# Kernel tuning notes

Hardware: AMD Instinct MI355X
Metric: run time of the kernel (lower is better)

Reference implementation:

```python
import jax, jax.numpy as jnp
import numpy as np

N = 100000        # num_nodes
W_IN = 256        # input feature dim
W_OUT = 64        # args.node_dim
C = 2             # args.num_channels
T = 4             # num_edge_type
E = 800000        # edges per edge type
NUM_CLASS = 4
M = 20000         # number of target nodes
BETA = 0.5        # args.beta


def setup_inputs() -> dict:
    key = jax.random.key(0)
    ks = jax.random.split(key, 10)
    X = jax.random.normal(ks[0], (N, W_IN), dtype=jnp.float32)
    edge_index = jax.random.randint(ks[1], (T, 2, E), 0, N)
    edge_value = jax.random.uniform(ks[2], (T, E), dtype=jnp.float32)
    target_x = jax.random.randint(ks[3], (M,), 0, N)
    target = jax.random.randint(ks[4], (M,), 0, NUM_CLASS)
    # learned params
    Ws = jax.random.normal(ks[5], (C, W_IN, W_OUT), dtype=jnp.float32) * 0.05   # GCNConv weights
    conv_weight = jax.random.normal(ks[6], (C, T), dtype=jnp.float32) * 0.1     # FastGTConv.weight
    linear1_W = jax.random.normal(ks[7], (W_OUT, W_OUT * C), dtype=jnp.float32) * 0.05
    linear1_b = jnp.zeros((W_OUT,), dtype=jnp.float32)
    lin_W = jax.random.normal(ks[8], (NUM_CLASS, W_OUT), dtype=jnp.float32) * 0.05
    lin_b = jnp.zeros((NUM_CLASS,), dtype=jnp.float32)
    return dict(X=X, edge_value=edge_value, Ws=Ws, conv_weight=conv_weight,
                linear1_W=linear1_W, linear1_b=linear1_b, lin_W=lin_W, lin_b=lin_b,
                edge_index=edge_index, target_x=target_x, target=target)


def reference(X, edge_value, Ws, conv_weight, linear1_W, linear1_b, lin_W, lin_b,
              edge_index, target_x, target):
    # FastGTConv: softmax over edge types per channel
    filt = jax.nn.softmax(conv_weight, axis=1)            # [C, T]
    rows = edge_index[:, 0, :].reshape(-1)                # [T*E]
    cols = edge_index[:, 1, :].reshape(-1)                # [T*E]
    # X_ = H = [X @ W_c for each channel]
    X_ = jnp.einsum('nd,cdo->cno', X, Ws)                 # [C, N, W_OUT]
    outs = []
    for c in range(C):
        # concat+coalesce(add) then spmm == scatter-add of weighted messages
        vals = (edge_value * filt[c][:, None]).reshape(-1)       # [T*E]
        msgs = vals[:, None] * X_[c][cols]                        # [T*E, W_OUT]
        Hc = jax.ops.segment_sum(msgs, rows, num_segments=N)      # [N, W_OUT]
        outs.append(jax.nn.relu(BETA * X_[c] + (1.0 - BETA) * Hc))
    H_ = jnp.concatenate(outs, axis=1)                    # [N, C*W_OUT]
    H_ = jax.nn.relu(H_ @ linear1_W.T + linear1_b)        # [N, W_OUT]
    y = H_[target_x] @ lin_W.T + lin_b                    # [M, NUM_CLASS]
    logp = jax.nn.log_softmax(y, axis=-1)
    loss = -jnp.mean(jnp.take_along_axis(logp, target[:, None], axis=1))
    return loss, y
```

## Files before the change

kernel.cpp:

```cpp
#include <hip/hip_runtime.h>

#define N_NODES 100000
#define W_INF   256
#define W_OUTF  64
#define C_CH    2
#define T_ET    4
#define E_EDGE  800000
#define NUM_CLS 4
#define M_TGT   20000
#define BETA    0.5f
#define MAXDEG  96

typedef __attribute__((ext_vector_type(8))) short bf16x8;
typedef __attribute__((ext_vector_type(4))) float floatx4;

__device__ inline short f2bf(float f) {
    unsigned u = __builtin_bit_cast(unsigned, f);
    u += 0x7FFF + ((u >> 16) & 1);
    return (short)(u >> 16);
}
__device__ inline float bflo(unsigned q) { return __builtin_bit_cast(float, q << 16); }
__device__ inline float bfhi(unsigned q) { return __builtin_bit_cast(float, q & 0xFFFF0000u); }

__global__ void setup_kernel(const float* __restrict__ Ws,
                             const float* __restrict__ conv_weight,
                             const int* __restrict__ target_x,
                             short* __restrict__ Bt, float* __restrict__ filt,
                             int* __restrict__ rid, int* __restrict__ nrows,
                             float* __restrict__ out) {
    int i = blockIdx.x * 256 + threadIdx.x;
    if (i == 0) { *nrows = 0; out[0] = 0.f; }
    if (i < C_CH) {
        int c = i;
        float mx = -1e30f;
        for (int t = 0; t < T_ET; t++) mx = fmaxf(mx, conv_weight[c * T_ET + t]);
        float e[T_ET];
        float s = 0.f;
        for (int t = 0; t < T_ET; t++) { e[t] = expf(conv_weight[c * T_ET + t] - mx); s += e[t]; }
        for (int t = 0; t < T_ET; t++) filt[c * T_ET + t] = e[t] / s;
    }
    if (i < C_CH * W_OUTF * W_INF) {
        int co = i >> 8, k = i & 255;
        int c = co >> 6, o = co & 63;
        Bt[i] = f2bf(Ws[((size_t)c * W_INF + k) * W_OUTF + o]);
    }
    if (i < M_TGT) rid[target_x[i]] = -2;
}

__global__ void compact_kernel(int* __restrict__ rid, int* __restrict__ row_list,
                               int* __restrict__ nrows, int* __restrict__ counts) {
    int n = blockIdx.x * blockDim.x + threadIdx.x;
    if (n < M_TGT) counts[n] = 0;
    int lane = threadIdx.x & 63;
    bool flag = (n < N_NODES) && (rid[n] == -2);
    unsigned long long mask = __ballot(flag);
    int base = 0;
    if (lane == 0 && mask) base = atomicAdd(nrows, __popcll(mask));
    base = __shfl(base, 0);
    if (flag) {
        int id = base + __popcll(mask & ((1ULL << lane) - 1ULL));
        rid[n] = id;
        row_list[id] = n;
    }
}

#define GMT  64
#define BLDA2 136
#define GEMM_NB  ((N_NODES + GMT - 1) / GMT)
#define BUILD_BX ((E_EDGE / 8 + 255) / 256)
#define BUILD_TOT (BUILD_BX * T_ET)
__global__ __launch_bounds__(256, 5)
void fused_gemm_build(const float* __restrict__ X, const short* __restrict__ Bt,
                      short* __restrict__ Xp,
                      const int* __restrict__ edge_index,
                      const float* __restrict__ edge_value,
                      const int* __restrict__ rid,
                      int* __restrict__ counts,
                      unsigned long long* __restrict__ records) {
    __shared__ short Bl[64][BLDA2];
    int tid = threadIdx.x;
    int bx = blockIdx.x;
    if ((bx & 1) == 0) {
        int g = bx >> 1;
        if (g >= GEMM_NB) return;
        int w = tid >> 6, lane = tid & 63;
        int quad = lane >> 4, l15 = lane & 15;
        int m0 = g * GMT + w * 16;
        int arow = m0 + l15;
        if (arow >= N_NODES) arow = N_NODES - 1;
        const float* xrow = X + (size_t)arow * W_INF;
        floatx4 acc[C_CH][4] = {};
        #pragma unroll 1
        for (int kh = 0; kh < 2; kh++) {
            bf16x8 af[4];
            #pragma unroll
            for (int kc = 0; kc < 4; kc++) {
                int kb = kh * 128 + kc * 32 + quad * 8;
                float4 v0 = *(const float4*)&xrow[kb];
                float4 v1 = *(const float4*)&xrow[kb + 4];
                af[kc][0] = f2bf(v0.x); af[kc][1] = f2bf(v0.y);
                af[kc][2] = f2bf(v0.z); af[kc][3] = f2bf(v0.w);
                af[kc][4] = f2bf(v1.x); af[kc][5] = f2bf(v1.y);
                af[kc][6] = f2bf(v1.z); af[kc][7] = f2bf(v1.w);
            }
            #pragma unroll
            for (int c = 0; c < C_CH; c++) {
                if (kh | c) __syncthreads();
                #pragma unroll
                for (int l = 0; l < 4; l++) {
                    int idx = tid + l * 256;
                    int r = idx >> 4;
                    int kp = (idx & 15) * 8;
                    *(bf16x8*)&Bl[r][kp] =
                        *(const bf16x8*)&Bt[(size_t)(c * 64 + r) * W_INF + kh * 128 + kp];
                }
                __syncthreads();
                #pragma unroll
                for (int kc = 0; kc < 4; kc++) {
                    int kb = kc * 32 + quad * 8;
                    #pragma unroll
                    for (int nt = 0; nt < 4; nt++) {
                        bf16x8 b = *(bf16x8*)&Bl[nt * 16 + l15][kb];
                        acc[c][nt] =
                            __builtin_amdgcn_mfma_f32_16x16x32_bf16(af[kc], b, acc[c][nt], 0, 0, 0);
                    }
                }
            }
        }
        #pragma unroll
        for (int nt = 0; nt < 4; nt++) {
            int o = nt * 16 + l15;
            #pragma unroll
            for (int r = 0; r < 4; r++) {
                int m = m0 + quad * 4 + r;
                if (m < N_NODES) {
                    unsigned pk = (unsigned)(unsigned short)f2bf(acc[0][nt][r])
                                | ((unsigned)(unsigned short)f2bf(acc[1][nt][r]) << 16);
                    *(unsigned*)&Xp[(size_t)m * (C_CH * W_OUTF) + o * 2] = pk;
                }
            }
        }
    } else {
        int bb = bx >> 1;
        if (bb >= BUILD_TOT) return;
        int t = bb / BUILD_BX;
        int i = (bb - t * BUILD_BX) * 256 + tid;
        if (i >= E_EDGE / 8) return;
        int e = i * 8;
        const int*   rbase = &edge_index[(size_t)(t * 2 + 0) * E_EDGE + e];
        const int*   cbase = &edge_index[(size_t)(t * 2 + 1) * E_EDGE + e];
        const float* vbase = &edge_value[(size_t)t * E_EDGE + e];
        int4   r4a = *(const int4*)  &rbase[0], r4b = *(const int4*)  &rbase[4];
        int4   c4a = *(const int4*)  &cbase[0], c4b = *(const int4*)  &cbase[4];
        float4 v4a = *(const float4*)&vbase[0], v4b = *(const float4*)&vbase[4];
        int rows[8] = {r4a.x, r4a.y, r4a.z, r4a.w, r4b.x, r4b.y, r4b.z, r4b.w};
        int cols[8] = {c4a.x, c4a.y, c4a.z, c4a.w, c4b.x, c4b.y, c4b.z, c4b.w};
        float evv[8] = {v4a.x, v4a.y, v4a.z, v4a.w, v4b.x, v4b.y, v4b.z, v4b.w};
        int ids[8];
        #pragma unroll
        for (int j = 0; j < 8; j++) ids[j] = rid[rows[j]];
        #pragma unroll
        for (int j = 0; j < 8; j++) {
            if (ids[j] >= 0) {
                int p = atomicAdd(&counts[ids[j]], 1);
                if (p < MAXDEG) {
                    unsigned long long rec =
                        (unsigned long long)(unsigned)(cols[j] | (t << 20)) |
                        ((unsigned long long)__float_as_uint(evv[j]) << 32);
                    records[(size_t)ids[j] * MAXDEG + p] = rec;
                }
            }
        }
    }
}

__global__ void gather_kernel(const int* __restrict__ row_list,
                              const int* __restrict__ counts,
                              const unsigned long long* __restrict__ records,
                              const float* __restrict__ filt,
                              const short* __restrict__ Xp,
                              float* __restrict__ Hcat,
                              const int* __restrict__ nrows_ptr) {
    int w = threadIdx.x >> 6, lane = threadIdx.x & 63;
    int b = blockIdx.x * 4 + w;
    if (b >= *nrows_ptr) return;
    float f0[T_ET], f1[T_ET];
    #pragma unroll
    for (int t = 0; t < T_ET; t++) { f0[t] = filt[t]; f1[t] = filt[T_ET + t]; }
    int n = row_list[b];
    int cnt = counts[b]; if (cnt > MAXDEG) cnt = MAXDEG;
    const unsigned long long* rec = records + (size_t)b * MAXDEG;
    unsigned long long rl = (lane < cnt)      ? rec[lane]      : 0ULL;
    unsigned long long rh = (lane + 64 < cnt) ? rec[lane + 64] : 0ULL;
    unsigned rl_lo = (unsigned)rl, rl_hi = (unsigned)(rl >> 32);
    unsigned rh_lo = (unsigned)rh, rh_hi = (unsigned)(rh >> 32);
    const unsigned* xb = (const unsigned*)Xp + lane;
    float a0 = 0.f, a1 = 0.f;
    int nb = (cnt + 15) & ~15;
    for (int p = 0; p < nb; p += 16) {
        unsigned blo = (p < 64) ? rl_lo : rh_lo;
        unsigned bhi = (p < 64) ? rl_hi : rh_hi;
        int poff = (p < 64) ? p : p - 64;
        unsigned klo[16], khi[16], q[16];
        #pragma unroll
        for (int j = 0; j < 16; j++) {
            klo[j] = __shfl(blo, poff + j);
            khi[j] = __shfl(bhi, poff + j);
        }
        #pragma unroll
        for (int j = 0; j < 16; j++)
            q[j] = xb[(size_t)(klo[j] & 0xFFFFF) * 64];
        #pragma unroll
        for (int j = 0; j < 16; j++) {
            int t = (int)(klo[j] >> 20);
            float e = __uint_as_float(khi[j]);
            a0 += e * f0[t] * bflo(q[j]);
            a1 += e * f1[t] * bfhi(q[j]);
        }
    }
    unsigned qn = xb[(size_t)n * 64];
    float h0 = BETA * bflo(qn) + (1.f - BETA) * a0;
    float h1 = BETA * bfhi(qn) + (1.f - BETA) * a1;
    Hcat[(size_t)b * (C_CH * W_OUTF) + lane]          = fmaxf(h0, 0.f);
    Hcat[(size_t)b * (C_CH * W_OUTF) + W_OUTF + lane] = fmaxf(h1, 0.f);
}

#define HTGT 80
__global__ void head_kernel(const float* __restrict__ Hcat,
                            const int* __restrict__ rid,
                            const float* __restrict__ W1,
                            const float* __restrict__ b1,
                            const float* __restrict__ linW,
                            const float* __restrict__ linb,
                            const int* __restrict__ target_x,
                            const int* __restrict__ target,
                            float* __restrict__ out) {
    __shared__ float w1s[C_CH * W_OUTF][W_OUTF + 1];
    __shared__ float hcat_s[4][C_CH * W_OUTF];
    __shared__ float loss_s[4];
    int tid = threadIdx.x;
    for (int i = tid; i < W_OUTF * C_CH * W_OUTF; i += 256) {
        int o = i >> 7, k = i & 127;
        w1s[k][o] = W1[i];
    }
    int wave = tid >> 6, lane = tid & 63;
    float l0 = linW[0 * W_OUTF + lane], l1 = linW[1 * W_OUTF + lane];
    float l2 = linW[2 * W_OUTF + lane], l3 = linW[3 * W_OUTF + lane];
    float lb0 = linb[0], lb1 = linb[1], lb2 = linb[2], lb3 = linb[3];
    float bias = b1[lane];
    float lsum = 0.f;
    __syncthreads();
    for (int it = 0; it < HTGT / 4; it++) {
        int m = blockIdx.x * HTGT + it * 4 + wave;
        int row = target_x[m];
        int id = rid[row];
        hcat_s[wave][lane]      = Hcat[(size_t)id * (C_CH * W_OUTF) + lane];
        hcat_s[wave][64 + lane] = Hcat[(size_t)id * (C_CH * W_OUTF) + 64 + lane];
        __syncthreads();
        float acc = bias;
        #pragma unroll 8
        for (int k = 0; k < C_CH * W_OUTF; k++) acc += hcat_s[wave][k] * w1s[k][lane];
        float h2 = fmaxf(acc, 0.f);
        float p0 = l0 * h2, p1 = l1 * h2, p2 = l2 * h2, p3 = l3 * h2;
        #pragma unroll
        for (int off = 32; off > 0; off >>= 1) {
            p0 += __shfl_xor(p0, off);
            p1 += __shfl_xor(p1, off);
            p2 += __shfl_xor(p2, off);
            p3 += __shfl_xor(p3, off);
        }
        if (lane == 0) {
            float y[NUM_CLS];
            y[0] = p0 + lb0; y[1] = p1 + lb1; y[2] = p2 + lb2; y[3] = p3 + lb3;
            float mx = fmaxf(fmaxf(y[0], y[1]), fmaxf(y[2], y[3]));
            float s = 0.f;
            #pragma unroll
            for (int k = 0; k < NUM_CLS; k++) s += expf(y[k] - mx);
            float lse = mx + logf(s);
            #pragma unroll
            for (int k = 0; k < NUM_CLS; k++) out[1 + (size_t)m * NUM_CLS + k] = y[k];
            int tg = target[m];
            lsum += lse - y[tg];
        }
        __syncthreads();
    }
    if (lane == 0) loss_s[wave] = lsum;
    __syncthreads();
    if (tid == 0) {
        float L = loss_s[0] + loss_s[1] + loss_s[2] + loss_s[3];
        atomicAdd(&out[0], L * (1.0f / (float)M_TGT));
    }
}

extern "C" void kernel_launch(void* const* d_in, const int* in_sizes, int n_in,
                              void* d_out, int out_size, void* d_ws, size_t ws_size,
                              hipStream_t stream) {
    const float* X           = (const float*)d_in[0];
    const float* edge_value  = (const float*)d_in[1];
    const float* Ws          = (const float*)d_in[2];
    const float* conv_weight = (const float*)d_in[3];
    const float* linear1_W   = (const float*)d_in[4];
    const float* linear1_b   = (const float*)d_in[5];
    const float* lin_W       = (const float*)d_in[6];
    const float* lin_b       = (const float*)d_in[7];
    const int*   edge_index  = (const int*)d_in[8];
    const int*   target_x    = (const int*)d_in[9];
    const int*   target      = (const int*)d_in[10];
    float* out = (float*)d_out;

    char* ws = (char*)d_ws;
    size_t off = 0;
    float* filt  = (float*)(ws + off); off += 256;
    size_t xbytes = (size_t)N_NODES * C_CH * W_OUTF * sizeof(short);
    short* Xp    = (short*)(ws + off); off += xbytes;
    float* Hcat  = (float*)(ws + off); off += (size_t)M_TGT * C_CH * W_OUTF * sizeof(float);
    unsigned long long* records = (unsigned long long*)(ws + off);
    off += (size_t)M_TGT * MAXDEG * sizeof(unsigned long long);
    short* Bt    = (short*)(ws + off); off += (size_t)C_CH * W_OUTF * W_INF * sizeof(short);
    int*   rid   = (int*)  (ws + off); off += (size_t)N_NODES * sizeof(int);
    int*   row_list = (int*)(ws + off); off += (size_t)M_TGT * sizeof(int);
    int*   counts   = (int*)(ws + off); off += (size_t)M_TGT * sizeof(int);
    int*   nrows    = (int*)(ws + off); off += 256;

    hipMemsetAsync(rid, 0xFF, (size_t)N_NODES * sizeof(int), stream);

    setup_kernel<<<128, 256, 0, stream>>>(Ws, conv_weight, target_x, Bt, filt, rid, nrows, out);
    compact_kernel<<<(N_NODES + 255) / 256, 256, 0, stream>>>(rid, row_list, nrows, counts);
    fused_gemm_build<<<2 * BUILD_TOT, 256, 0, stream>>>(
        X, Bt, Xp, edge_index, edge_value, rid, counts, records);
    gather_kernel<<<(M_TGT + 3) / 4, 256, 0, stream>>>(row_list, counts, records, filt, Xp, Hcat, nrows);
    head_kernel<<<M_TGT / HTGT, 256, 0, stream>>>(Hcat, rid, linear1_W, linear1_b, lin_W, lin_b,
                                                  target_x, target, out);
}
```

Baseline: 323.4 us.

## Fuse linear1 projection into gather kernel and simplify head kernel

```diff
diff --git a/kernel.cpp b/kernel.cpp
--- a/kernel.cpp
+++ b/kernel.cpp
@@ -69,7 +69,7 @@
 #define GEMM_NB  ((N_NODES + GMT - 1) / GMT)
 #define BUILD_BX ((E_EDGE / 8 + 255) / 256)
 #define BUILD_TOT (BUILD_BX * T_ET)
-__global__ __launch_bounds__(256, 5)
+__global__ __launch_bounds__(256, 4)
 void fused_gemm_build(const float* __restrict__ X, const short* __restrict__ Bt,
                       short* __restrict__ Xp,
                       const int* __restrict__ edge_index,
@@ -174,93 +174,97 @@
     }
 }
 
+#define GROWS 16
 __global__ void gather_kernel(const int* __restrict__ row_list,
                               const int* __restrict__ counts,
                               const unsigned long long* __restrict__ records,
                               const float* __restrict__ filt,
                               const short* __restrict__ Xp,
-                              float* __restrict__ Hcat,
+                              const float* __restrict__ W1,
+                              const float* __restrict__ b1,
+                              float* __restrict__ H2,
                               const int* __restrict__ nrows_ptr) {
-    int w = threadIdx.x >> 6, lane = threadIdx.x & 63;
-    int b = blockIdx.x * 4 + w;
-    if (b >= *nrows_ptr) return;
+    __shared__ float w1s[C_CH * W_OUTF][W_OUTF + 1];
+    int tid = threadIdx.x;
+    for (int i = tid; i < W_OUTF * C_CH * W_OUTF; i += 256) {
+        int o = i >> 7, k = i & 127;
+        w1s[k][o] = W1[i];
+    }
+    __syncthreads();
+    int w = tid >> 6, lane = tid & 63;
+    int nrows = *nrows_ptr;
     float f0[T_ET], f1[T_ET];
     #pragma unroll
     for (int t = 0; t < T_ET; t++) { f0[t] = filt[t]; f1[t] = filt[T_ET + t]; }
-    int n = row_list[b];
-    int cnt = counts[b]; if (cnt > MAXDEG) cnt = MAXDEG;
-    const unsigned long long* rec = records + (size_t)b * MAXDEG;
-    unsigned long long rl = (lane < cnt)      ? rec[lane]      : 0ULL;
-    unsigned long long rh = (lane + 64 < cnt) ? rec[lane + 64] : 0ULL;
-    unsigned rl_lo = (unsigned)rl, rl_hi = (unsigned)(rl >> 32);
-    unsigned rh_lo = (unsigned)rh, rh_hi = (unsigned)(rh >> 32);
+    float bias = b1[lane];
     const unsigned* xb = (const unsigned*)Xp + lane;
-    float a0 = 0.f, a1 = 0.f;
-    int nb = (cnt + 15) & ~15;
-    for (int p = 0; p < nb; p += 16) {
-        unsigned blo = (p < 64) ? rl_lo : rh_lo;
-        unsigned bhi = (p < 64) ? rl_hi : rh_hi;
-        int poff = (p < 64) ? p : p - 64;
-        unsigned klo[16], khi[16], q[16];
-        #pragma unroll
-        for (int j = 0; j < 16; j++) {
-            klo[j] = __shfl(blo, poff + j);
-            khi[j] = __shfl(bhi, poff + j);
-        }
-        #pragma unroll
-        for (int j = 0; j < 16; j++)
-            q[j] = xb[(size_t)(klo[j] & 0xFFFFF) * 64];
-        #pragma unroll
-        for (int j = 0; j < 16; j++) {
-            int t = (int)(klo[j] >> 20);
-            float e = __uint_as_float(khi[j]);
-            a0 += e * f0[t] * bflo(q[j]);
-            a1 += e * f1[t] * bfhi(q[j]);
-        }
-    }
-    unsigned qn = xb[(size_t)n * 64];
-    float h0 = BETA * bflo(qn) + (1.f - BETA) * a0;
-    float h1 = BETA * bfhi(qn) + (1.f - BETA) * a1;
-    Hcat[(size_t)b * (C_CH * W_OUTF) + lane]          = fmaxf(h0, 0.f);
-    Hcat[(size_t)b * (C_CH * W_OUTF) + W_OUTF + lane] = fmaxf(h1, 0.f);
-}
-
-#define HTGT 80
-__global__ void head_kernel(const float* __restrict__ Hcat,
+    for (int it = 0; it < GROWS / 4; it++) {
+        int b = blockIdx.x * GROWS + it * 4 + w;
+        if (b >= nrows) continue;
+        int n = row_list[b];
+        int cnt = counts[b]; if (cnt > MAXDEG) cnt = MAXDEG;
+        const unsigned long long* rec = records + (size_t)b * MAXDEG;
+        unsigned long long rl = (lane < cnt)      ? rec[lane]      : 0ULL;
+        unsigned long long rh = (lane + 64 < cnt) ? rec[lane + 64] : 0ULL;
+        unsigned rl_lo = (unsigned)rl, rl_hi = (unsigned)(rl >> 32);
+        unsigned rh_lo = (unsigned)rh, rh_hi = (unsigned)(rh >> 32);
+        float a0 = 0.f, a1 = 0.f;
+        int nb = (cnt + 15) & ~15;
+        for (int p = 0; p < nb; p += 16) {
+            unsigned blo = (p < 64) ? rl_lo : rh_lo;
+            unsigned bhi = (p < 64) ? rl_hi : rh_hi;
+            int poff = (p < 64) ? p : p - 64;
+            unsigned klo[16], khi[16], q[16];
+            #pragma unroll
+            for (int j = 0; j < 16; j++) {
+                klo[j] = __shfl(blo, poff + j);
+                khi[j] = __shfl(bhi, poff + j);
+            }
+            #pragma unroll
+            for (int j = 0; j < 16; j++)
+                q[j] = xb[(size_t)(klo[j] & 0xFFFFF) * 64];
+            #pragma unroll
+            for (int j = 0; j < 16; j++) {
+                int t = (int)(klo[j] >> 20);
+                float e = __uint_as_float(khi[j]);
+                a0 += e * f0[t] * bflo(q[j]);
+                a1 += e * f1[t] * bfhi(q[j]);
+            }
+        }
+        unsigned qn = xb[(size_t)n * 64];
+        float hc0 = fmaxf(BETA * bflo(qn) + (1.f - BETA) * a0, 0.f);
+        float hc1 = fmaxf(BETA * bfhi(qn) + (1.f - BETA) * a1, 0.f);
+        float acc = bias;
+        #pragma unroll
+        for (int k = 0; k < W_OUTF; k++)
+            acc += __shfl(hc0, k) * w1s[k][lane];
+        #pragma unroll
+        for (int k = 0; k < W_OUTF; k++)
+            acc += __shfl(hc1, k) * w1s[W_OUTF + k][lane];
+        H2[(size_t)b * W_OUTF + lane] = fmaxf(acc, 0.f);
+    }
+}
+
+#define HTGT 32
+__global__ void head_kernel(const float* __restrict__ H2,
                             const int* __restrict__ rid,
-                            const float* __restrict__ W1,
-                            const float* __restrict__ b1,
                             const float* __restrict__ linW,
                             const float* __restrict__ linb,
                             const int* __restrict__ target_x,
                             const int* __restrict__ target,
                             float* __restrict__ out) {
-    __shared__ float w1s[C_CH * W_OUTF][W_OUTF + 1];
-    __shared__ float hcat_s[4][C_CH * W_OUTF];
     __shared__ float loss_s[4];
     int tid = threadIdx.x;
-    for (int i = tid; i < W_OUTF * C_CH * W_OUTF; i += 256) {
-        int o = i >> 7, k = i & 127;
-        w1s[k][o] = W1[i];
-    }
     int wave = tid >> 6, lane = tid & 63;
     float l0 = linW[0 * W_OUTF + lane], l1 = linW[1 * W_OUTF + lane];
     float l2 = linW[2 * W_OUTF + lane], l3 = linW[3 * W_OUTF + lane];
     float lb0 = linb[0], lb1 = linb[1], lb2 = linb[2], lb3 = linb[3];
-    float bias = b1[lane];
     float lsum = 0.f;
-    __syncthreads();
     for (int it = 0; it < HTGT / 4; it++) {
         int m = blockIdx.x * HTGT + it * 4 + wave;
         int row = target_x[m];
         int id = rid[row];
-        hcat_s[wave][lane]      = Hcat[(size_t)id * (C_CH * W_OUTF) + lane];
-        hcat_s[wave][64 + lane] = Hcat[(size_t)id * (C_CH * W_OUTF) + 64 + lane];
-        __syncthreads();
-        float acc = bias;
-        #pragma unroll 8
-        for (int k = 0; k < C_CH * W_OUTF; k++) acc += hcat_s[wave][k] * w1s[k][lane];
-        float h2 = fmaxf(acc, 0.f);
+        float h2 = H2[(size_t)id * W_OUTF + lane];
         float p0 = l0 * h2, p1 = l1 * h2, p2 = l2 * h2, p3 = l3 * h2;
         #pragma unroll
         for (int off = 32; off > 0; off >>= 1) {
@@ -282,7 +286,6 @@
             int tg = target[m];
             lsum += lse - y[tg];
         }
-        __syncthreads();
     }
     if (lane == 0) loss_s[wave] = lsum;
     __syncthreads();
@@ -313,7 +316,7 @@
     float* filt  = (float*)(ws + off); off += 256;
     size_t xbytes = (size_t)N_NODES * C_CH * W_OUTF * sizeof(short);
     short* Xp    = (short*)(ws + off); off += xbytes;
-    float* Hcat  = (float*)(ws + off); off += (size_t)M_TGT * C_CH * W_OUTF * sizeof(float);
+    float* H2    = (float*)(ws + off); off += (size_t)M_TGT * W_OUTF * sizeof(float);
     unsigned long long* records = (unsigned long long*)(ws + off);
     off += (size_t)M_TGT * MAXDEG * sizeof(unsigned long long);
     short* Bt    = (short*)(ws + off); off += (size_t)C_CH * W_OUTF * W_INF * sizeof(short);
@@ -328,7 +331,8 @@
     compact_kernel<<<(N_NODES + 255) / 256, 256, 0, stream>>>(rid, row_list, nrows, counts);
     fused_gemm_build<<<2 * BUILD_TOT, 256, 0, stream>>>(
         X, Bt, Xp, edge_index, edge_value, rid, counts, records);
-    gather_kernel<<<(M_TGT + 3) / 4, 256, 0, stream>>>(row_list, counts, records, filt, Xp, Hcat, nrows);
-    head_kernel<<<M_TGT / HTGT, 256, 0, stream>>>(Hcat, rid, linear1_W, linear1_b, lin_W, lin_b,
+    gather_kernel<<<(M_TGT + GROWS - 1) / GROWS, 256, 0, stream>>>(
+        row_list, counts, records, filt, Xp, linear1_W, linear1_b, H2, nrows);
+    head_kernel<<<M_TGT / HTGT, 256, 0, stream>>>(H2, rid, lin_W, lin_b,
                                                   target_x, target, out);
 }
```

Measured after the change: 330.9 us. 2.3% more time.
